# Kernel optimization log

Hardware: AMD Instinct MI355X
Metric: run time of the kernel (lower is better)

Reference implementation:

```python
import jax, jax.numpy as jnp
import numpy as np

N, E, B = 50000, 800000, 16
IN_DIM, ED, HD, SD, NC = 64, 8, 128, 128, 8
T_STEPS = (8 + 16) // 2  # eval mode: (t_min + t_max) // 2 = 12


def setup_inputs() -> dict:
    key = jax.random.key(0)
    ks = jax.random.split(key, 12)
    s = 0.05  # small init scale so 12 residual steps stay bounded
    return {
        "x": jax.random.normal(ks[0], (N, IN_DIM), jnp.float32),
        "edge_index": jax.random.randint(ks[1], (2, E), 0, N, jnp.int64),
        "edge_attr": jax.random.normal(ks[2], (E, ED), jnp.float32),
        "batch": jnp.sort(jax.random.randint(ks[3], (N,), 0, B, jnp.int64)),
        "enc_w": jax.random.normal(ks[4], (IN_DIM, SD), jnp.float32) * s,
        "enc_b": jnp.zeros((SD,), jnp.float32),
        "msg_w": jax.random.normal(ks[5], (SD + ED, HD), jnp.float32) * s,
        "msg_b": jnp.zeros((HD,), jnp.float32),
        "up_w1": jax.random.normal(ks[6], (SD + HD, HD), jnp.float32) * s,
        "up_b1": jnp.zeros((HD,), jnp.float32),
        "up_w2": jax.random.normal(ks[7], (HD, SD), jnp.float32) * s,
        "up_b2": jnp.zeros((SD,), jnp.float32),
    }


def reference(x, edge_index, edge_attr, batch, enc_w, enc_b, msg_w, msg_b,
              up_w1, up_b1, up_w2, up_b2):
    src, dst = edge_index[0], edge_index[1]  # x_j = x[src], aggregate at dst
    # in-degree for mean aggregation (zero-degree nodes get 0, clamp avoids /0)
    deg = jax.ops.segment_sum(jnp.ones((E,), x.dtype), dst, num_segments=N)
    deg = jnp.clip(deg, 1.0)[:, None]

    # Encoder: Linear + ReLU
    state = jax.nn.relu(x @ enc_w + enc_b)  # [N, SD]

    for _ in range(T_STEPS):
        # message: relu(W_msg @ [h_j || e_ji])
        m = jax.nn.relu(jnp.concatenate([state[src], edge_attr], axis=-1) @ msg_w + msg_b)  # [E, HD]
        agg = jax.ops.segment_sum(m, dst, num_segments=N) / deg  # scatter-mean [N, HD]
        # update MLP on [h_i || m_bar_i]
        h = jax.nn.relu(jnp.concatenate([state, agg], axis=-1) @ up_w1 + up_b1)
        delta = h @ up_w2 + up_b2
        state = state + delta  # eval: no stochastic mask, no noise

    # Readout: per-graph mean over class channels
    class_ch = state[:, -NC:]  # [N, NC]
    cnt = jax.ops.segment_sum(jnp.ones((N,), x.dtype), batch, num_segments=B)
    logits = jax.ops.segment_sum(class_ch, batch, num_segments=B) / jnp.clip(cnt, 1.0)[:, None]
    return logits
```

## Files before the change

kernel.cpp:

```cpp
#include <hip/hip_runtime.h>
#include <hip/hip_bf16.h>

#define NN 50000
#define NE 800000
#define NB 16
#define T_STEPS 12
#define SCAN_B 196
#define EAW_BLOCKS 2048

typedef __attribute__((ext_vector_type(8))) short short8;
typedef __attribute__((ext_vector_type(4))) float f32x4;
typedef __attribute__((ext_vector_type(2))) float f32x2;
typedef unsigned short u16;
typedef unsigned int u32;

__device__ __forceinline__ float bf2f(u32 u) {
    union { u32 i; float f; } v; v.i = u << 16; return v.f;
}
__device__ __forceinline__ u16 f2bf(float f) {
    union { float f; u32 i; } v; v.f = f;
    u32 r = v.i + 0x7fffu + ((v.i >> 16) & 1u);
    return (u16)(r >> 16);
}
__device__ __forceinline__ f32x4 mfma16(short8 a, short8 b, f32x4 c) {
    return __builtin_amdgcn_mfma_f32_16x16x32_bf16(a, b, c, 0, 0, 0);
}

__device__ __forceinline__ u32 pk2_fp8(float o0, float o1) {
#if __has_builtin(__builtin_amdgcn_cvt_pk_fp8_f32)
    return (u32)__builtin_amdgcn_cvt_pk_fp8_f32(o0, o1, 0, false);
#else
    u32 a = 0;
    asm("v_cvt_pk_fp8_f32 %0, %1, %2" : "+v"(a) : "v"(o0), "v"(o1));
    return a;
#endif
}
__device__ __forceinline__ u32 pk4_fp8(float o0, float o1, float o2, float o3) {
    return (pk2_fp8(o0, o1) & 0xffffu) | (pk2_fp8(o2, o3) << 16);
}

__device__ __forceinline__ void fp8x4f(u32 w, float& f0, float& f1, float& f2, float& f3) {
#if __has_builtin(__builtin_amdgcn_cvt_pk_f32_fp8)
    f32x2 r0 = __builtin_amdgcn_cvt_pk_f32_fp8((int)w, false);
    f32x2 r1 = __builtin_amdgcn_cvt_pk_f32_fp8((int)w, true);
    f0 = r0[0]; f1 = r0[1]; f2 = r1[0]; f3 = r1[1];
#else
    f32x2 r0, r1;
    u32 hi = w >> 16;
    asm("v_cvt_pk_f32_fp8 %0, %1" : "=v"(r0) : "v"(w));
    asm("v_cvt_pk_f32_fp8 %0, %1" : "=v"(r1) : "v"(hi));
    f0 = r0[0]; f1 = r0[1]; f2 = r1[0]; f3 = r1[1];
#endif
}

#define W1OFF 0
#define W2OFF 32768
#define WSOFF 49152
#define ENCOFF 65536
#define PACKN 73728


__global__ void k_hist(const int* __restrict__ dst, int* __restrict__ hist) {
    int e = blockIdx.x * 256 + threadIdx.x;
    if (e < NE) atomicAdd(&hist[dst[e]], 1);
}

__global__ void k_scanA(const int* __restrict__ hist, int* __restrict__ excl,
                        int* __restrict__ bsum) {
    __shared__ int sh[256];
    int t = threadIdx.x, b = blockIdx.x;
    int idx = b * 256 + t;
    int v = (idx < NN) ? hist[idx] : 0;
    sh[t] = v;
    __syncthreads();
    for (int off = 1; off < 256; off <<= 1) {
        int add = (t >= off) ? sh[t - off] : 0;
        __syncthreads();
        sh[t] += add;
        __syncthreads();
    }
    if (idx < NN) excl[idx] = sh[t] - v;
    if (t == 255) bsum[b] = sh[255];
}

__global__ void k_scanB(int* __restrict__ bsum) {
    __shared__ int sh[256];
    int t = threadIdx.x;
    int v = (t < SCAN_B) ? bsum[t] : 0;
    sh[t] = v;
    __syncthreads();
    for (int off = 1; off < 256; off <<= 1) {
        int add = (t >= off) ? sh[t - off] : 0;
        __syncthreads();
        sh[t] += add;
        __syncthreads();
    }
    if (t < SCAN_B) bsum[t] = sh[t] - v;
}

__global__ void k_scanC(const int* __restrict__ excl, const int* __restrict__ bsum,
                        int* __restrict__ rowptr, int* __restrict__ cursor) {
    int idx = blockIdx.x * 256 + threadIdx.x;
    if (idx < NN) {
        int r = excl[idx] + bsum[blockIdx.x];
        rowptr[idx] = r;
        cursor[idx] = r;
    }
    if (idx == 0) rowptr[NN] = NE;
}

__global__ void k_scatter(const int* __restrict__ src, const int* __restrict__ dst,
                          int* __restrict__ cursor, int* __restrict__ ssrc,
                          int* __restrict__ seid) {
    int e = blockIdx.x * 256 + threadIdx.x;
    if (e >= NE) return;
    int d = dst[e];
    int pos = atomicAdd(&cursor[d], 1);
    ssrc[pos] = src[e];
    seid[pos] = e;
}

__global__ __launch_bounds__(256) void k_eaw(
    const int* __restrict__ seid, const float* __restrict__ eattr,
    const float* __restrict__ msg_w, unsigned char* __restrict__ eaw) {
    __shared__ float elds[256][8];
    const int tid = threadIdx.x;
    const int hex = tid & 15;
    const int esub = tid >> 4;
    float w[8][8];
#pragma unroll
    for (int k = 0; k < 8; ++k) {
        float4 v0 = *(const float4*)(msg_w + (size_t)(128 + k) * 128 + hex * 8);
        float4 v1 = *(const float4*)(msg_w + (size_t)(128 + k) * 128 + hex * 8 + 4);
        w[k][0] = v0.x; w[k][1] = v0.y; w[k][2] = v0.z; w[k][3] = v0.w;
        w[k][4] = v1.x; w[k][5] = v1.y; w[k][6] = v1.z; w[k][7] = v1.w;
    }
    for (int p0 = blockIdx.x * 256; p0 < NE; p0 += EAW_BLOCKS * 256) {
        __syncthreads();
        int p = p0 + tid;
        if (p < NE) {
            int eid = seid[p];
            const float* ar = eattr + (size_t)eid * 8;
            float4 a0 = *(const float4*)ar;
            float4 a1 = *(const float4*)(ar + 4);
            *(float4*)&elds[tid][0] = a0;
            *(float4*)&elds[tid][4] = a1;
        }
        __syncthreads();
#pragma unroll 4
        for (int j = 0; j < 16; ++j) {
            int idx = esub + j * 16;
            int pp = p0 + idx;
            if (pp >= NE) continue;
            float4 a0 = *(const float4*)&elds[idx][0];
            float4 a1 = *(const float4*)&elds[idx][4];
            float ef[8] = {a0.x, a0.y, a0.z, a0.w, a1.x, a1.y, a1.z, a1.w};
            float o[8];
#pragma unroll
            for (int c = 0; c < 8; ++c) o[c] = ef[0] * w[0][c];
#pragma unroll
            for (int k = 1; k < 8; ++k)
#pragma unroll
                for (int c = 0; c < 8; ++c) o[c] += ef[k] * w[k][c];
            uint2 q;
            q.x = pk4_fp8(o[0], o[1], o[2], o[3]);
            q.y = pk4_fp8(o[4], o[5], o[6], o[7]);
            *(uint2*)(eaw + (size_t)pp * 128 + hex * 8) = q;
        }
    }
}

__global__ void k_pack(const float* __restrict__ up_w1, const float* __restrict__ up_w2,
                       const float* __restrict__ msg_w, const float* __restrict__ enc_w,
                       u16* __restrict__ packed) {
    int idx = blockIdx.x * 256 + threadIdx.x;
    if (idx >= PACKN) return;
    const float* srcp; int local;
    if (idx < W2OFF)        { srcp = up_w1; local = idx; }
    else if (idx < WSOFF)   { srcp = up_w2; local = idx - W2OFF; }
    else if (idx < ENCOFF)  { srcp = msg_w; local = idx - WSOFF; }
    else                    { srcp = enc_w; local = idx - ENCOFF; }
    int j = local & 7;
    int l = (local >> 3) & 63;
    int ntks = local >> 9;
    int nt = ntks & 7;
    int ks = ntks >> 3;
    int krow = ks * 32 + (l >> 4) * 8 + j;
    int col = nt * 16 + (l & 15);
    packed[idx] = f2bf(srcp[krow * 128 + col]);
}


__global__ __launch_bounds__(256) void k_encode(
    const float* __restrict__ x, const float* __restrict__ enc_b,
    const float* __restrict__ msg_b, const u16* __restrict__ packed,
    float* __restrict__ state_f, u16* __restrict__ state_h, u16* __restrict__ swb) {
    __shared__ u16 stage[4][2048];
    const int wv = threadIdx.x >> 6, l = threadIdx.x & 63;
    const int lr = l & 15, kb = l >> 4;
    const int rb = blockIdx.x * 64 + wv * 16;
    const int row = rb + lr;
    const int rowc = row < NN ? row : NN - 1;

    f32x4 acc[8] = {};
#pragma unroll
    for (int ks = 0; ks < 2; ++ks) {
        const float* ap = x + (size_t)rowc * 64 + ks * 32 + kb * 8;
        float4 a0 = *(const float4*)ap;
        float4 a1 = *(const float4*)(ap + 4);
        short8 a;
        a[0] = (short)f2bf(a0.x); a[1] = (short)f2bf(a0.y);
        a[2] = (short)f2bf(a0.z); a[3] = (short)f2bf(a0.w);
        a[4] = (short)f2bf(a1.x); a[5] = (short)f2bf(a1.y);
        a[6] = (short)f2bf(a1.z); a[7] = (short)f2bf(a1.w);
        const u16* bp = packed + ENCOFF + (size_t)(ks * 512 + l) * 8;
#pragma unroll
        for (int nt = 0; nt < 8; ++nt) {
            short8 b = *(const short8*)(bp + nt * 512);
            acc[nt] = mfma16(a, b, acc[nt]);
        }
    }
#pragma unroll
    for (int nt = 0; nt < 8; ++nt) {
        int col = nt * 16 + lr;
        float bias = enc_b[col];
#pragma unroll
        for (int j = 0; j < 4; ++j) {
            int rl = kb * 4 + j;
            int r = rb + rl;
            float v = acc[nt][j] + bias;
            v = v > 0.f ? v : 0.f;
            u16 h = f2bf(v);
            if (r < NN) {
                state_f[(size_t)r * 128 + col] = v;
                state_h[(size_t)r * 128 + col] = h;
            }
            int byte = (rl * 256 + col * 2) ^ ((rl & 7) << 4);
            *(u16*)((char*)stage[wv] + byte) = h;
        }
    }
    f32x4 acc3[8] = {};
#pragma unroll
    for (int ks = 0; ks < 4; ++ks) {
        int byte = (lr * 256 + ks * 64 + kb * 16) ^ ((lr & 7) << 4);
        short8 a = *(const short8*)((char*)stage[wv] + byte);
        const u16* bp = packed + WSOFF + (size_t)(ks * 512 + l) * 8;
#pragma unroll
        for (int nt = 0; nt < 8; ++nt) {
            short8 b = *(const short8*)(bp + nt * 512);
            acc3[nt] = mfma16(a, b, acc3[nt]);
        }
    }
#pragma unroll
    for (int nt = 0; nt < 8; ++nt) {
        int col = nt * 16 + lr;
        float bias = msg_b[col];
#pragma unroll
        for (int j = 0; j < 4; ++j) {
            int r = rb + kb * 4 + j;
            if (r < NN) swb[(size_t)r * 128 + col] = f2bf(acc3[nt][j] + bias);
        }
    }
}


__global__ __launch_bounds__(256) void k_edge(
    const int* __restrict__ rowptr, const int* __restrict__ ssrc,
    const unsigned char* __restrict__ eaw, const u16* __restrict__ swb,
    u16* __restrict__ aggb) {
    __shared__ float red[4][2][4][129];
    const int wv = threadIdx.x >> 6, l = threadIdx.x & 63;
    const int half = l >> 5;
    const int slot = (l >> 3) & 3;
    const int g = l & 7;
    const int n = blockIdx.x * 8 + wv * 2 + half;
    if (n >= NN) return;
    const int e0 = rowptr[n], e1 = rowptr[n + 1];
    float acc[16];
#pragma unroll
    for (int c = 0; c < 16; ++c) acc[c] = 0.f;

    int i = e0 + slot;
    int s = (i < e1) ? ssrc[i] : 0;
    while (i < e1) {
        int inext = i + 4;
        int snext = (inext < e1) ? ssrc[inext] : 0;
        uint4 q = *(const uint4*)(eaw + (size_t)i * 128 + g * 16);
        const u16* sp = swb + (size_t)s * 128 + g * 16;
        uint4 sa = *(const uint4*)sp;
        uint4 sb = *(const uint4*)(sp + 8);
        float ef[16];
        fp8x4f(q.x, ef[0], ef[1], ef[2], ef[3]);
        fp8x4f(q.y, ef[4], ef[5], ef[6], ef[7]);
        fp8x4f(q.z, ef[8], ef[9], ef[10], ef[11]);
        fp8x4f(q.w, ef[12], ef[13], ef[14], ef[15]);
        u32 sw[8] = {sa.x, sa.y, sa.z, sa.w, sb.x, sb.y, sb.z, sb.w};
#pragma unroll
        for (int h = 0; h < 8; ++h) {
            union { u32 i; float f; } vlo, vhi;
            vlo.i = sw[h] << 16;
            vhi.i = sw[h] & 0xffff0000u;
            float m0 = vlo.f + ef[2 * h];
            float m1 = vhi.f + ef[2 * h + 1];
            acc[2 * h]     += m0 > 0.f ? m0 : 0.f;
            acc[2 * h + 1] += m1 > 0.f ? m1 : 0.f;
        }
        i = inext;
        s = snext;
    }
    float* rp = &red[wv][half][slot][g * 16];
#pragma unroll
    for (int c = 0; c < 16; c += 4) {
        f32x4 v = {acc[c], acc[c + 1], acc[c + 2], acc[c + 3]};
        *(f32x4*)(rp + c) = v;
    }
    const int lo = l & 31;
    const int ch = lo * 4;
    f32x4 sum = *(const f32x4*)&red[wv][half][0][ch];
#pragma unroll
    for (int sl = 1; sl < 4; ++sl) {
        f32x4 v = *(const f32x4*)&red[wv][half][sl][ch];
        sum[0] += v[0]; sum[1] += v[1]; sum[2] += v[2]; sum[3] += v[3];
    }
    int dg = e1 - e0;
    float inv = 1.f / (float)(dg > 0 ? dg : 1);
    uint2 outw;
    outw.x = (u32)f2bf(sum[0] * inv) | ((u32)f2bf(sum[1] * inv) << 16);
    outw.y = (u32)f2bf(sum[2] * inv) | ((u32)f2bf(sum[3] * inv) << 16);
    *(uint2*)(aggb + (size_t)n * 128 + ch) = outw;
}


__global__ __launch_bounds__(256) void k_update(
    const float* __restrict__ up_b1, const float* __restrict__ up_b2,
    const float* __restrict__ msg_b, const u16* __restrict__ packed,
    const u16* __restrict__ aggb, float* __restrict__ state_f,
    u16* __restrict__ state_h, u16* __restrict__ swb) {
    __shared__ u16 stage[4][2][2048];
    const int wv = threadIdx.x >> 6, l = threadIdx.x & 63;
    const int lr = l & 15, kb = l >> 4;
    const int rbase = blockIdx.x * 128 + wv * 32;

    f32x4 acc[2][8] = {};
#pragma unroll
    for (int ks = 0; ks < 8; ++ks) {
        short8 a[2];
#pragma unroll
        for (int rt = 0; rt < 2; ++rt) {
            int row = rbase + rt * 16 + lr;
            int rowc = row < NN ? row : NN - 1;
            const u16* abase = (ks < 4)
                ? (state_h + (size_t)rowc * 128 + ks * 32 + kb * 8)
                : (aggb + (size_t)rowc * 128 + (ks - 4) * 32 + kb * 8);
            a[rt] = *(const short8*)abase;
        }
        const u16* bp = packed + W1OFF + (size_t)(ks * 512 + l) * 8;
#pragma unroll
        for (int nt = 0; nt < 8; ++nt) {
            short8 b = *(const short8*)(bp + nt * 512);
            acc[0][nt] = mfma16(a[0], b, acc[0][nt]);
            acc[1][nt] = mfma16(a[1], b, acc[1][nt]);
        }
    }
#pragma unroll
    for (int nt = 0; nt < 8; ++nt) {
        int col = nt * 16 + lr;
        float b1v = up_b1[col];
#pragma unroll
        for (int rt = 0; rt < 2; ++rt) {
#pragma unroll
            for (int j = 0; j < 4; ++j) {
                int rl = kb * 4 + j;
                float v = acc[rt][nt][j] + b1v;
                v = v > 0.f ? v : 0.f;
                int byte = (rl * 256 + col * 2) ^ ((rl & 7) << 4);
                *(u16*)((char*)stage[wv][rt] + byte) = f2bf(v);
            }
        }
    }
    f32x4 acc2[2][8] = {};
#pragma unroll
    for (int ks = 0; ks < 4; ++ks) {
        int byte = (lr * 256 + ks * 64 + kb * 16) ^ ((lr & 7) << 4);
        short8 a[2];
        a[0] = *(const short8*)((char*)stage[wv][0] + byte);
        a[1] = *(const short8*)((char*)stage[wv][1] + byte);
        const u16* bp = packed + W2OFF + (size_t)(ks * 512 + l) * 8;
#pragma unroll
        for (int nt = 0; nt < 8; ++nt) {
            short8 b = *(const short8*)(bp + nt * 512);
            acc2[0][nt] = mfma16(a[0], b, acc2[0][nt]);
            acc2[1][nt] = mfma16(a[1], b, acc2[1][nt]);
        }
    }
#pragma unroll
    for (int rt = 0; rt < 2; ++rt) {
#pragma unroll
        for (int nt = 0; nt < 8; ++nt) {
            int col = nt * 16 + lr;
            float b2v = up_b2[col];
#pragma unroll
            for (int j = 0; j < 4; ++j) {
                int rl = kb * 4 + j;
                int r = rbase + rt * 16 + rl;
                int rc = r < NN ? r : NN - 1;
                float snew = state_f[(size_t)rc * 128 + col] + acc2[rt][nt][j] + b2v;
                u16 hb = f2bf(snew);
                if (r < NN) {
                    state_f[(size_t)r * 128 + col] = snew;
                    state_h[(size_t)r * 128 + col] = hb;
                }
                int byte = (rl * 256 + col * 2) ^ ((rl & 7) << 4);
                *(u16*)((char*)stage[wv][rt] + byte) = hb;
            }
        }
    }
    f32x4 acc3[2][8] = {};
#pragma unroll
    for (int ks = 0; ks < 4; ++ks) {
        int byte = (lr * 256 + ks * 64 + kb * 16) ^ ((lr & 7) << 4);
        short8 a[2];
        a[0] = *(const short8*)((char*)stage[wv][0] + byte);
        a[1] = *(const short8*)((char*)stage[wv][1] + byte);
        const u16* bp = packed + WSOFF + (size_t)(ks * 512 + l) * 8;
#pragma unroll
        for (int nt = 0; nt < 8; ++nt) {
            short8 b = *(const short8*)(bp + nt * 512);
            acc3[0][nt] = mfma16(a[0], b, acc3[0][nt]);
            acc3[1][nt] = mfma16(a[1], b, acc3[1][nt]);
        }
    }
#pragma unroll
    for (int rt = 0; rt < 2; ++rt) {
#pragma unroll
        for (int nt = 0; nt < 8; ++nt) {
            int col = nt * 16 + lr;
            float bias = msg_b[col];
#pragma unroll
            for (int j = 0; j < 4; ++j) {
                int r = rbase + rt * 16 + kb * 4 + j;
                if (r < NN) swb[(size_t)r * 128 + col] = f2bf(acc3[rt][nt][j] + bias);
            }
        }
    }
}


__global__ void k_logits(const float* __restrict__ state_f, const int* __restrict__ batch,
                         float* __restrict__ out) {
    __shared__ float red[256];
    int b = blockIdx.x, t = threadIdx.x;
    int ch = t & 7, sub = t >> 3;
    int lo = 0, hi = NN;
    while (lo < hi) { int m = (lo + hi) >> 1; if (batch[m] < b) lo = m + 1; else hi = m; }
    int s0 = lo;
    lo = 0; hi = NN;
    while (lo < hi) { int m = (lo + hi) >> 1; if (batch[m] < b + 1) lo = m + 1; else hi = m; }
    int s1 = lo;
    float acc = 0.f;
    for (int n = s0 + sub; n < s1; n += 32)
        acc += state_f[(size_t)n * 128 + 120 + ch];
    red[t] = acc;
    __syncthreads();
    for (int off = 16; off >= 1; off >>= 1) {
        if (sub < off) red[t] += red[t + off * 8];
        __syncthreads();
    }
    if (sub == 0) {
        int c = s1 - s0;
        float cnt = (float)(c > 0 ? c : 1);
        out[b * 8 + ch] = red[ch] / cnt;
    }
}


extern "C" void kernel_launch(void* const* d_in, const int* in_sizes, int n_in,
                              void* d_out, int out_size, void* d_ws, size_t ws_size,
                              hipStream_t stream) {
    (void)in_sizes; (void)n_in;
    const float* x      = (const float*)d_in[0];
    const int*   eidx   = (const int*)d_in[1];
    const float* eattr  = (const float*)d_in[2];
    const int*   batch  = (const int*)d_in[3];
    const float* enc_w  = (const float*)d_in[4];
    const float* enc_b  = (const float*)d_in[5];
    const float* msg_w  = (const float*)d_in[6];
    const float* msg_b  = (const float*)d_in[7];
    const float* up_w1  = (const float*)d_in[8];
    const float* up_b1  = (const float*)d_in[9];
    const float* up_w2  = (const float*)d_in[10];
    const float* up_b2  = (const float*)d_in[11];
    const int* esrc = eidx;
    const int* edst = eidx + NE;

    char* p = (char*)d_ws;
    size_t off = 0;
    auto carve = [&](size_t bytes) -> char* {
        char* r = p + off;
        off += (bytes + 255) & ~(size_t)255;
        return r;
    };
    float* state_f = (float*)carve((size_t)NN * 128 * 4);
    u16* state_h   = (u16*)carve((size_t)NN * 128 * 2);
    u16* aggb      = (u16*)carve((size_t)NN * 128 * 2);
    u16* swb       = (u16*)carve((size_t)NN * 128 * 2);
    int* ssrc      = (int*)carve((size_t)NE * 4);
    int* seid      = (int*)carve((size_t)NE * 4);
    unsigned char* eaw = (unsigned char*)carve((size_t)NE * 128);
    int* rowptr    = (int*)carve((size_t)(NN + 1) * 4);
    int* cursor    = (int*)carve((size_t)NN * 4);
    int* hist      = (int*)carve((size_t)NN * 4);
    int* sexcl     = (int*)carve((size_t)NN * 4);
    int* bsum      = (int*)carve((size_t)256 * 4);
    u16* packed    = (u16*)carve((size_t)PACKN * 2);
    if (off > ws_size) {
        hipMemsetAsync(d_out, 0xFF, (size_t)out_size * 4, stream);
        return;
    }

    hipMemsetAsync(hist, 0, (size_t)NN * 4, stream);
    k_hist<<<(NE + 255) / 256, 256, 0, stream>>>(edst, hist);
    k_scanA<<<SCAN_B, 256, 0, stream>>>(hist, sexcl, bsum);
    k_scanB<<<1, 256, 0, stream>>>(bsum);
    k_scanC<<<SCAN_B, 256, 0, stream>>>(sexcl, bsum, rowptr, cursor);
    k_scatter<<<(NE + 255) / 256, 256, 0, stream>>>(esrc, edst, cursor, ssrc, seid);
    k_eaw<<<EAW_BLOCKS, 256, 0, stream>>>(seid, eattr, msg_w, eaw);
    k_pack<<<(PACKN + 255) / 256, 256, 0, stream>>>(up_w1, up_w2, msg_w, enc_w, packed);
    k_encode<<<(NN + 63) / 64, 256, 0, stream>>>(x, enc_b, msg_b, packed, state_f, state_h, swb);
    for (int t = 0; t < T_STEPS; ++t) {
        k_edge<<<(NN + 7) / 8, 256, 0, stream>>>(rowptr, ssrc, eaw, swb, aggb);
        k_update<<<(NN + 127) / 128, 256, 0, stream>>>(up_b1, up_b2, msg_b, packed, aggb,
                                                       state_f, state_h, swb);
    }
    k_logits<<<NB, 256, 0, stream>>>(state_f, batch, (float*)d_out);
}
```

Baseline: 1.210 ms.

## Fuse edge aggregation and node update into one per-step kernel with ping-pong buffers

Merges the per-step edge gather/aggregate kernel and the update MLP kernel into a single k_step kernel. Each wave aggregates 16 nodes into LDS, then runs the MFMA update on them, so the aggregate buffer no longer makes a global round trip. The projected message buffer is double-buffered so it can be read and written in the same launch. Also packs src and edge id into an int2 and gives k_eaw one block per 256 edges. The risk is lower parallelism in the gather phase (one wave walks 16 nodes in turn, 8 edge slots each) and smaller M-tiles in the update, which could cost more than the saved traffic and launches.

```diff
diff --git a/kernel.cpp b/kernel.cpp
--- a/kernel.cpp
+++ b/kernel.cpp
@@ -6,7 +6,6 @@
 #define NB 16
 #define T_STEPS 12
 #define SCAN_B 196
-#define EAW_BLOCKS 2048
 
 typedef __attribute__((ext_vector_type(8))) short short8;
 typedef __attribute__((ext_vector_type(4))) float f32x4;
@@ -110,18 +109,17 @@
 }
 
 __global__ void k_scatter(const int* __restrict__ src, const int* __restrict__ dst,
-                          int* __restrict__ cursor, int* __restrict__ ssrc,
-                          int* __restrict__ seid) {
+                          int* __restrict__ cursor, int2* __restrict__ sse) {
     int e = blockIdx.x * 256 + threadIdx.x;
     if (e >= NE) return;
     int d = dst[e];
     int pos = atomicAdd(&cursor[d], 1);
-    ssrc[pos] = src[e];
-    seid[pos] = e;
+    int2 v; v.x = src[e]; v.y = e;
+    sse[pos] = v;
 }
 
 __global__ __launch_bounds__(256) void k_eaw(
-    const int* __restrict__ seid, const float* __restrict__ eattr,
+    const int2* __restrict__ sse, const float* __restrict__ eattr,
     const float* __restrict__ msg_w, unsigned char* __restrict__ eaw) {
     __shared__ float elds[256][8];
     const int tid = threadIdx.x;
@@ -135,38 +133,33 @@
         w[k][0] = v0.x; w[k][1] = v0.y; w[k][2] = v0.z; w[k][3] = v0.w;
         w[k][4] = v1.x; w[k][5] = v1.y; w[k][6] = v1.z; w[k][7] = v1.w;
     }
-    for (int p0 = blockIdx.x * 256; p0 < NE; p0 += EAW_BLOCKS * 256) {
-        __syncthreads();
-        int p = p0 + tid;
-        if (p < NE) {
-            int eid = seid[p];
-            const float* ar = eattr + (size_t)eid * 8;
-            float4 a0 = *(const float4*)ar;
-            float4 a1 = *(const float4*)(ar + 4);
-            *(float4*)&elds[tid][0] = a0;
-            *(float4*)&elds[tid][4] = a1;
-        }
-        __syncthreads();
+    const int p0 = blockIdx.x * 256;
+    {
+        int eid = sse[p0 + tid].y;
+        const float* ar = eattr + (size_t)eid * 8;
+        float4 a0 = *(const float4*)ar;
+        float4 a1 = *(const float4*)(ar + 4);
+        *(float4*)&elds[tid][0] = a0;
+        *(float4*)&elds[tid][4] = a1;
+    }
+    __syncthreads();
 #pragma unroll 4
-        for (int j = 0; j < 16; ++j) {
-            int idx = esub + j * 16;
-            int pp = p0 + idx;
-            if (pp >= NE) continue;
-            float4 a0 = *(const float4*)&elds[idx][0];
-            float4 a1 = *(const float4*)&elds[idx][4];
-            float ef[8] = {a0.x, a0.y, a0.z, a0.w, a1.x, a1.y, a1.z, a1.w};
-            float o[8];
-#pragma unroll
-            for (int c = 0; c < 8; ++c) o[c] = ef[0] * w[0][c];
-#pragma unroll
-            for (int k = 1; k < 8; ++k)
-#pragma unroll
-                for (int c = 0; c < 8; ++c) o[c] += ef[k] * w[k][c];
-            uint2 q;
-            q.x = pk4_fp8(o[0], o[1], o[2], o[3]);
-            q.y = pk4_fp8(o[4], o[5], o[6], o[7]);
-            *(uint2*)(eaw + (size_t)pp * 128 + hex * 8) = q;
-        }
+    for (int j = 0; j < 16; ++j) {
+        int idx = esub + j * 16;
+        float4 a0 = *(const float4*)&elds[idx][0];
+        float4 a1 = *(const float4*)&elds[idx][4];
+        float ef[8] = {a0.x, a0.y, a0.z, a0.w, a1.x, a1.y, a1.z, a1.w};
+        float o[8];
+#pragma unroll
+        for (int c = 0; c < 8; ++c) o[c] = ef[0] * w[0][c];
+#pragma unroll
+        for (int k = 1; k < 8; ++k)
+#pragma unroll
+            for (int c = 0; c < 8; ++c) o[c] += ef[k] * w[k][c];
+        uint2 q;
+        q.x = pk4_fp8(o[0], o[1], o[2], o[3]);
+        q.y = pk4_fp8(o[4], o[5], o[6], o[7]);
+        *(uint2*)(eaw + (size_t)(p0 + idx) * 128 + hex * 8) = q;
     }
 }
 
@@ -264,102 +257,99 @@
 }
 
 
-__global__ __launch_bounds__(256) void k_edge(
-    const int* __restrict__ rowptr, const int* __restrict__ ssrc,
-    const unsigned char* __restrict__ eaw, const u16* __restrict__ swb,
-    u16* __restrict__ aggb) {
-    __shared__ float red[4][2][4][129];
-    const int wv = threadIdx.x >> 6, l = threadIdx.x & 63;
-    const int half = l >> 5;
-    const int slot = (l >> 3) & 3;
-    const int g = l & 7;
-    const int n = blockIdx.x * 8 + wv * 2 + half;
-    if (n >= NN) return;
-    const int e0 = rowptr[n], e1 = rowptr[n + 1];
-    float acc[16];
-#pragma unroll
-    for (int c = 0; c < 16; ++c) acc[c] = 0.f;
-
-    int i = e0 + slot;
-    int s = (i < e1) ? ssrc[i] : 0;
-    while (i < e1) {
-        int inext = i + 4;
-        int snext = (inext < e1) ? ssrc[inext] : 0;
-        uint4 q = *(const uint4*)(eaw + (size_t)i * 128 + g * 16);
-        const u16* sp = swb + (size_t)s * 128 + g * 16;
-        uint4 sa = *(const uint4*)sp;
-        uint4 sb = *(const uint4*)(sp + 8);
-        float ef[16];
-        fp8x4f(q.x, ef[0], ef[1], ef[2], ef[3]);
-        fp8x4f(q.y, ef[4], ef[5], ef[6], ef[7]);
-        fp8x4f(q.z, ef[8], ef[9], ef[10], ef[11]);
-        fp8x4f(q.w, ef[12], ef[13], ef[14], ef[15]);
-        u32 sw[8] = {sa.x, sa.y, sa.z, sa.w, sb.x, sb.y, sb.z, sb.w};
-#pragma unroll
-        for (int h = 0; h < 8; ++h) {
-            union { u32 i; float f; } vlo, vhi;
-            vlo.i = sw[h] << 16;
-            vhi.i = sw[h] & 0xffff0000u;
-            float m0 = vlo.f + ef[2 * h];
-            float m1 = vhi.f + ef[2 * h + 1];
-            acc[2 * h]     += m0 > 0.f ? m0 : 0.f;
-            acc[2 * h + 1] += m1 > 0.f ? m1 : 0.f;
-        }
-        i = inext;
-        s = snext;
-    }
-    float* rp = &red[wv][half][slot][g * 16];
-#pragma unroll
-    for (int c = 0; c < 16; c += 4) {
-        f32x4 v = {acc[c], acc[c + 1], acc[c + 2], acc[c + 3]};
-        *(f32x4*)(rp + c) = v;
-    }
-    const int lo = l & 31;
-    const int ch = lo * 4;
-    f32x4 sum = *(const f32x4*)&red[wv][half][0][ch];
-#pragma unroll
-    for (int sl = 1; sl < 4; ++sl) {
-        f32x4 v = *(const f32x4*)&red[wv][half][sl][ch];
-        sum[0] += v[0]; sum[1] += v[1]; sum[2] += v[2]; sum[3] += v[3];
-    }
-    int dg = e1 - e0;
-    float inv = 1.f / (float)(dg > 0 ? dg : 1);
-    uint2 outw;
-    outw.x = (u32)f2bf(sum[0] * inv) | ((u32)f2bf(sum[1] * inv) << 16);
-    outw.y = (u32)f2bf(sum[2] * inv) | ((u32)f2bf(sum[3] * inv) << 16);
-    *(uint2*)(aggb + (size_t)n * 128 + ch) = outw;
-}
-
-
-__global__ __launch_bounds__(256) void k_update(
+#define STEP_SMEM_PER_WAVE 8224
+
+__global__ __launch_bounds__(256) void k_step(
+    const int* __restrict__ rowptr, const int2* __restrict__ sse,
+    const unsigned char* __restrict__ eaw, const u16* __restrict__ swb_in,
     const float* __restrict__ up_b1, const float* __restrict__ up_b2,
     const float* __restrict__ msg_b, const u16* __restrict__ packed,
-    const u16* __restrict__ aggb, float* __restrict__ state_f,
-    u16* __restrict__ state_h, u16* __restrict__ swb) {
-    __shared__ u16 stage[4][2][2048];
+    float* __restrict__ state_f, u16* __restrict__ state_h,
+    u16* __restrict__ swb_out) {
+    __shared__ char smem[4 * STEP_SMEM_PER_WAVE];
     const int wv = threadIdx.x >> 6, l = threadIdx.x & 63;
+    char* wbase = smem + wv * STEP_SMEM_PER_WAVE;
+    u16* aggl = (u16*)wbase;
+    float* red = (float*)(wbase + 4096);
+    u16* stage = (u16*)(wbase + 4096);
+    const int rbase = blockIdx.x * 64 + wv * 16;
+
+    {
+        const int slot = l >> 3, g = l & 7;
+        for (int nl = 0; nl < 16; ++nl) {
+            int n = rbase + nl;
+            int nc = n < NN ? n : NN - 1;
+            int e0 = rowptr[nc], e1 = rowptr[nc + 1];
+            float acc[16];
+#pragma unroll
+            for (int c = 0; c < 16; ++c) acc[c] = 0.f;
+            int i = e0 + slot;
+            int s = (i < e1) ? sse[i].x : 0;
+            while (i < e1) {
+                int inext = i + 8;
+                int snext = (inext < e1) ? sse[inext].x : 0;
+                uint4 q = *(const uint4*)(eaw + (size_t)i * 128 + g * 16);
+                const u16* sp = swb_in + (size_t)s * 128 + g * 16;
+                uint4 sa = *(const uint4*)sp;
+                uint4 sb = *(const uint4*)(sp + 8);
+                float ef[16];
+                fp8x4f(q.x, ef[0], ef[1], ef[2], ef[3]);
+                fp8x4f(q.y, ef[4], ef[5], ef[6], ef[7]);
+                fp8x4f(q.z, ef[8], ef[9], ef[10], ef[11]);
+                fp8x4f(q.w, ef[12], ef[13], ef[14], ef[15]);
+                u32 sw[8] = {sa.x, sa.y, sa.z, sa.w, sb.x, sb.y, sb.z, sb.w};
+#pragma unroll
+                for (int h = 0; h < 8; ++h) {
+                    union { u32 i; float f; } vlo, vhi;
+                    vlo.i = sw[h] << 16;
+                    vhi.i = sw[h] & 0xffff0000u;
+                    float m0 = vlo.f + ef[2 * h];
+                    float m1 = vhi.f + ef[2 * h + 1];
+                    acc[2 * h]     += m0 > 0.f ? m0 : 0.f;
+                    acc[2 * h + 1] += m1 > 0.f ? m1 : 0.f;
+                }
+                i = inext;
+                s = snext;
+            }
+            float* rp = red + slot * 129 + g * 16;
+#pragma unroll
+            for (int c = 0; c < 16; c += 4) {
+                f32x4 v = {acc[c], acc[c + 1], acc[c + 2], acc[c + 3]};
+                *(f32x4*)(rp + c) = v;
+            }
+            float v0 = 0.f, v1 = 0.f;
+#pragma unroll
+            for (int sl = 0; sl < 8; ++sl) {
+                v0 += red[sl * 129 + l * 2];
+                v1 += red[sl * 129 + l * 2 + 1];
+            }
+            int dg = e1 - e0;
+            float inv = 1.f / (float)(dg > 0 ? dg : 1);
+            u32 outw = (u32)f2bf(v0 * inv) | ((u32)f2bf(v1 * inv) << 16);
+            int byte = (nl * 256 + l * 4) ^ ((nl & 7) << 4);
+            *(u32*)((char*)aggl + byte) = outw;
+        }
+    }
+
     const int lr = l & 15, kb = l >> 4;
-    const int rbase = blockIdx.x * 128 + wv * 32;
-
-    f32x4 acc[2][8] = {};
+    const int row = rbase + lr;
+    const int rowc = row < NN ? row : NN - 1;
+
+    f32x4 acc1[8] = {};
 #pragma unroll
     for (int ks = 0; ks < 8; ++ks) {
-        short8 a[2];
-#pragma unroll
-        for (int rt = 0; rt < 2; ++rt) {
-            int row = rbase + rt * 16 + lr;
-            int rowc = row < NN ? row : NN - 1;
-            const u16* abase = (ks < 4)
-                ? (state_h + (size_t)rowc * 128 + ks * 32 + kb * 8)
-                : (aggb + (size_t)rowc * 128 + (ks - 4) * 32 + kb * 8);
-            a[rt] = *(const short8*)abase;
+        short8 a;
+        if (ks < 4) {
+            a = *(const short8*)(state_h + (size_t)rowc * 128 + ks * 32 + kb * 8);
+        } else {
+            int byte = (lr * 256 + (ks - 4) * 64 + kb * 16) ^ ((lr & 7) << 4);
+            a = *(const short8*)((char*)aggl + byte);
         }
         const u16* bp = packed + W1OFF + (size_t)(ks * 512 + l) * 8;
 #pragma unroll
         for (int nt = 0; nt < 8; ++nt) {
             short8 b = *(const short8*)(bp + nt * 512);
-            acc[0][nt] = mfma16(a[0], b, acc[0][nt]);
-            acc[1][nt] = mfma16(a[1], b, acc[1][nt]);
+            acc1[nt] = mfma16(a, b, acc1[nt]);
         }
     }
 #pragma unroll
@@ -367,80 +357,65 @@
         int col = nt * 16 + lr;
         float b1v = up_b1[col];
 #pragma unroll
-        for (int rt = 0; rt < 2; ++rt) {
-#pragma unroll
-            for (int j = 0; j < 4; ++j) {
-                int rl = kb * 4 + j;
-                float v = acc[rt][nt][j] + b1v;
-                v = v > 0.f ? v : 0.f;
-                int byte = (rl * 256 + col * 2) ^ ((rl & 7) << 4);
-                *(u16*)((char*)stage[wv][rt] + byte) = f2bf(v);
-            }
-        }
-    }
-    f32x4 acc2[2][8] = {};
+        for (int j = 0; j < 4; ++j) {
+            int rl = kb * 4 + j;
+            float v = acc1[nt][j] + b1v;
+            v = v > 0.f ? v : 0.f;
+            int byte = (rl * 256 + col * 2) ^ ((rl & 7) << 4);
+            *(u16*)((char*)stage + byte) = f2bf(v);
+        }
+    }
+    f32x4 acc2[8] = {};
 #pragma unroll
     for (int ks = 0; ks < 4; ++ks) {
         int byte = (lr * 256 + ks * 64 + kb * 16) ^ ((lr & 7) << 4);
-        short8 a[2];
-        a[0] = *(const short8*)((char*)stage[wv][0] + byte);
-        a[1] = *(const short8*)((char*)stage[wv][1] + byte);
+        short8 a = *(const short8*)((char*)stage + byte);
         const u16* bp = packed + W2OFF + (size_t)(ks * 512 + l) * 8;
 #pragma unroll
         for (int nt = 0; nt < 8; ++nt) {
             short8 b = *(const short8*)(bp + nt * 512);
-            acc2[0][nt] = mfma16(a[0], b, acc2[0][nt]);
-            acc2[1][nt] = mfma16(a[1], b, acc2[1][nt]);
-        }
-    }
-#pragma unroll
-    for (int rt = 0; rt < 2; ++rt) {
-#pragma unroll
-        for (int nt = 0; nt < 8; ++nt) {
-            int col = nt * 16 + lr;
-            float b2v = up_b2[col];
-#pragma unroll
-            for (int j = 0; j < 4; ++j) {
-                int rl = kb * 4 + j;
-                int r = rbase + rt * 16 + rl;
-                int rc = r < NN ? r : NN - 1;
-                float snew = state_f[(size_t)rc * 128 + col] + acc2[rt][nt][j] + b2v;
-                u16 hb = f2bf(snew);
-                if (r < NN) {
-                    state_f[(size_t)r * 128 + col] = snew;
-                    state_h[(size_t)r * 128 + col] = hb;
-                }
-                int byte = (rl * 256 + col * 2) ^ ((rl & 7) << 4);
-                *(u16*)((char*)stage[wv][rt] + byte) = hb;
+            acc2[nt] = mfma16(a, b, acc2[nt]);
+        }
+    }
+#pragma unroll
+    for (int nt = 0; nt < 8; ++nt) {
+        int col = nt * 16 + lr;
+        float b2v = up_b2[col];
+#pragma unroll
+        for (int j = 0; j < 4; ++j) {
+            int rl = kb * 4 + j;
+            int r = rbase + rl;
+            int rc = r < NN ? r : NN - 1;
+            float snew = state_f[(size_t)rc * 128 + col] + acc2[nt][j] + b2v;
+            u16 hb = f2bf(snew);
+            if (r < NN) {
+                state_f[(size_t)r * 128 + col] = snew;
+                state_h[(size_t)r * 128 + col] = hb;
             }
-        }
-    }
-    f32x4 acc3[2][8] = {};
+            int byte = (rl * 256 + col * 2) ^ ((rl & 7) << 4);
+            *(u16*)((char*)stage + byte) = hb;
+        }
+    }
+    f32x4 acc3[8] = {};
 #pragma unroll
     for (int ks = 0; ks < 4; ++ks) {
         int byte = (lr * 256 + ks * 64 + kb * 16) ^ ((lr & 7) << 4);
-        short8 a[2];
-        a[0] = *(const short8*)((char*)stage[wv][0] + byte);
-        a[1] = *(const short8*)((char*)stage[wv][1] + byte);
+        short8 a = *(const short8*)((char*)stage + byte);
         const u16* bp = packed + WSOFF + (size_t)(ks * 512 + l) * 8;
 #pragma unroll
         for (int nt = 0; nt < 8; ++nt) {
             short8 b = *(const short8*)(bp + nt * 512);
-            acc3[0][nt] = mfma16(a[0], b, acc3[0][nt]);
-            acc3[1][nt] = mfma16(a[1], b, acc3[1][nt]);
-        }
-    }
-#pragma unroll
-    for (int rt = 0; rt < 2; ++rt) {
-#pragma unroll
-        for (int nt = 0; nt < 8; ++nt) {
-            int col = nt * 16 + lr;
-            float bias = msg_b[col];
-#pragma unroll
-            for (int j = 0; j < 4; ++j) {
-                int r = rbase + rt * 16 + kb * 4 + j;
-                if (r < NN) swb[(size_t)r * 128 + col] = f2bf(acc3[rt][nt][j] + bias);
-            }
+            acc3[nt] = mfma16(a, b, acc3[nt]);
+        }
+    }
+#pragma unroll
+    for (int nt = 0; nt < 8; ++nt) {
+        int col = nt * 16 + lr;
+        float bias = msg_b[col];
+#pragma unroll
+        for (int j = 0; j < 4; ++j) {
+            int r = rbase + kb * 4 + j;
+            if (r < NN) swb_out[(size_t)r * 128 + col] = f2bf(acc3[nt][j] + bias);
         }
     }
 }
@@ -502,10 +477,9 @@
     };
     float* state_f = (float*)carve((size_t)NN * 128 * 4);
     u16* state_h   = (u16*)carve((size_t)NN * 128 * 2);
-    u16* aggb      = (u16*)carve((size_t)NN * 128 * 2);
-    u16* swb       = (u16*)carve((size_t)NN * 128 * 2);
-    int* ssrc      = (int*)carve((size_t)NE * 4);
-    int* seid      = (int*)carve((size_t)NE * 4);
+    u16* swb0      = (u16*)carve((size_t)NN * 128 * 2);
+    u16* swb1      = (u16*)carve((size_t)NN * 128 * 2);
+    int2* sse      = (int2*)carve((size_t)NE * 8);
     unsigned char* eaw = (unsigned char*)carve((size_t)NE * 128);
     int* rowptr    = (int*)carve((size_t)(NN + 1) * 4);
     int* cursor    = (int*)carve((size_t)NN * 4);
@@ -523,14 +497,17 @@
     k_scanA<<<SCAN_B, 256, 0, stream>>>(hist, sexcl, bsum);
     k_scanB<<<1, 256, 0, stream>>>(bsum);
     k_scanC<<<SCAN_B, 256, 0, stream>>>(sexcl, bsum, rowptr, cursor);
-    k_scatter<<<(NE + 255) / 256, 256, 0, stream>>>(esrc, edst, cursor, ssrc, seid);
-    k_eaw<<<EAW_BLOCKS, 256, 0, stream>>>(seid, eattr, msg_w, eaw);
+    k_scatter<<<(NE + 255) / 256, 256, 0, stream>>>(esrc, edst, cursor, sse);
+    k_eaw<<<NE / 256, 256, 0, stream>>>(sse, eattr, msg_w, eaw);
     k_pack<<<(PACKN + 255) / 256, 256, 0, stream>>>(up_w1, up_w2, msg_w, enc_w, packed);
-    k_encode<<<(NN + 63) / 64, 256, 0, stream>>>(x, enc_b, msg_b, packed, state_f, state_h, swb);
+    k_encode<<<(NN + 63) / 64, 256, 0, stream>>>(x, enc_b, msg_b, packed, state_f, state_h, swb0);
+    u16* sin = swb0;
+    u16* sout = swb1;
     for (int t = 0; t < T_STEPS; ++t) {
-        k_edge<<<(NN + 7) / 8, 256, 0, stream>>>(rowptr, ssrc, eaw, swb, aggb);
-        k_update<<<(NN + 127) / 128, 256, 0, stream>>>(up_b1, up_b2, msg_b, packed, aggb,
-                                                       state_f, state_h, swb);
+        k_step<<<(NN + 63) / 64, 256, 0, stream>>>(rowptr, sse, eaw, sin,
+                                                   up_b1, up_b2, msg_b, packed,
+                                                   state_f, state_h, sout);
+        u16* tmp = sin; sin = sout; sout = tmp;
     }
     k_logits<<<NB, 256, 0, stream>>>(state_f, batch, (float*)d_out);
 }
```

New measurement: 1.633 ms. 35.0% more time.
